# Optimization experiments

Hardware: AMD Instinct MI355X
Metric: run time of the kernel (lower is better)

The kernel has to match this reference:

```python
import jax, jax.numpy as jnp
import numpy as np

SIZE = (96, 160, 160)  # (D, H, W) from init_kwargs


def grid_sample_3d(inp, grid, padding_mode):
    """PyTorch-semantics 3D grid_sample, trilinear, align_corners=True.
    inp: (B, C, D, H, W); grid: (B, Do, Ho, Wo, 3) with grid[...,0]=x(W), [...,1]=y(H), [...,2]=z(D).
    """
    B, C, D, H, W = inp.shape
    x = (grid[..., 0] + 1.0) * 0.5 * (W - 1)
    y = (grid[..., 1] + 1.0) * 0.5 * (H - 1)
    z = (grid[..., 2] + 1.0) * 0.5 * (D - 1)
    if padding_mode == 'border':
        x = jnp.clip(x, 0.0, W - 1)
        y = jnp.clip(y, 0.0, H - 1)
        z = jnp.clip(z, 0.0, D - 1)
    x0f, y0f, z0f = jnp.floor(x), jnp.floor(y), jnp.floor(z)
    fx, fy, fz = x - x0f, y - y0f, z - z0f
    x0, y0, z0 = x0f.astype(jnp.int32), y0f.astype(jnp.int32), z0f.astype(jnp.int32)
    x1, y1, z1 = x0 + 1, y0 + 1, z0 + 1

    flat = inp.reshape(B, C, D * H * W)
    Do, Ho, Wo = grid.shape[1:4]
    N = Do * Ho * Wo

    def corner(zi, yi, xi, w):
        if padding_mode == 'zeros':
            valid = ((zi >= 0) & (zi < D) & (yi >= 0) & (yi < H) & (xi >= 0) & (xi < W))
            w = w * valid.astype(inp.dtype)
        zi = jnp.clip(zi, 0, D - 1)
        yi = jnp.clip(yi, 0, H - 1)
        xi = jnp.clip(xi, 0, W - 1)
        idx = ((zi * H + yi) * W + xi).reshape(B, 1, N)
        vals = jnp.take_along_axis(flat, idx, axis=2).reshape(B, C, Do, Ho, Wo)
        return vals * w[:, None]

    out = (corner(z0, y0, x0, (1 - fz) * (1 - fy) * (1 - fx))
           + corner(z0, y0, x1, (1 - fz) * (1 - fy) * fx)
           + corner(z0, y1, x0, (1 - fz) * fy * (1 - fx))
           + corner(z0, y1, x1, (1 - fz) * fy * fx)
           + corner(z1, y0, x0, fz * (1 - fy) * (1 - fx))
           + corner(z1, y0, x1, fz * (1 - fy) * fx)
           + corner(z1, y1, x0, fz * fy * (1 - fx))
           + corner(z1, y1, x1, fz * fy * fx))
    return out


def make_grid():
    D, H, W = SIZE
    g = jnp.stack(jnp.meshgrid(jnp.arange(D), jnp.arange(H), jnp.arange(W), indexing='ij'))
    return g[None].astype(jnp.float32)  # (1, 3, D, H, W)


def setup_inputs() -> dict:
    key = jax.random.key(0)
    k1, k2 = jax.random.split(key)
    D, H, W = SIZE
    src = jax.random.normal(k1, (1, 1, D, H, W), dtype=jnp.float32)
    flows = jax.random.normal(k2, (3, 1, 3, D, H, W), dtype=jnp.float32)
    range_flow = jnp.float32(0.4)
    return {"src": src, "flows": flows, "range_flow": range_flow}


def reference(src, flows, range_flow):
    D, H, W = SIZE
    grid = make_grid()  # (1, 3, D, H, W)
    shape = jnp.array([D, H, W], dtype=jnp.float32).reshape(-1, 1, 1, 1)
    acc = jnp.zeros_like(grid)
    for i in range(flows.shape[0]):  # small fixed number of flow stages
        flow = flows[i]
        ng = 2.0 * (grid / shape) - 1.0
        warped = grid_sample_3d(flow, jnp.transpose(ng, (0, 2, 3, 4, 1)), 'border')
        acc = acc + warped
    final = grid + acc * range_flow
    denom = jnp.array([D - 1, H - 1, W - 1], dtype=jnp.float32).reshape(-1, 1, 1, 1)
    final = 2.0 * (final / denom - 0.5)
    fg = jnp.transpose(final, (0, 2, 3, 4, 1))
    return grid_sample_3d(src, fg, 'zeros')
```

## Files before the change

kernel.cpp:

```cpp
#include <hip/hip_runtime.h>
#include <stdint.h>

constexpr int Dz = 96, Hy = 160, Wx = 160;
constexpr int NVOX = Dz * Hy * Wx;

constexpr int ZW = 6, YW = 3, XP = 56;
constexpr int ROWS = ZW * YW;
constexpr int NCHUNK = ROWS * 14;
constexpr int UI = 4;
constexpr int WBUF = UI * 64 * 4;

typedef __attribute__((address_space(3))) float lds_f;
typedef __attribute__((address_space(1))) const void gbl_v;

#define WAIT_VM(N)  do { asm volatile("s_waitcnt vmcnt(" #N ")" ::: "memory"); \
                         __builtin_amdgcn_sched_barrier(0); } while (0)
#define WAIT_LGKM() do { asm volatile("s_waitcnt lgkmcnt(0)" ::: "memory"); \
                         __builtin_amdgcn_sched_barrier(0); } while (0)

__global__ __launch_bounds__(128) void st_fused_kernel(
    const float* __restrict__ src,
    const float* __restrict__ flows,
    const float* __restrict__ rfp,
    float* __restrict__ out)
{
    __shared__ float raw[2][2][WBUF];
    const int t = threadIdx.x;
    const int v = t >> 6;
    const int lane = t & 63;

    const int bid = blockIdx.x;
    const int swz = (bid & 7) * 300 + (bid >> 3);
    const int wid = swz * 2 + v;
    const int wt = wid % 20;
    const int rest = wid / 20;
    const int dt = rest % 3;
    const int hp = rest / 3;
    const int w0w = wt * 8, d0 = dt * 32, h0 = hp * 2;
    const float rf = *rfp;

    const int Z0w = (19 * w0w) >> 5;
    const int X0 = 53 * dt;
    const int X0a = X0 & ~3;
    const int YB = (159 * h0) / 160;

    const char* ap[UI];
    {
        const char* fb = (const char*)flows + ((size_t)YB * Wx + X0a) * 4;
#pragma unroll
        for (int u = 0; u < UI; ++u) {
            int c = u * 64 + lane;
            if (c >= NCHUNK) c = NCHUNK - 1;
            int row = c / 14, ch = c - row * 14;
            int zr = row / 3, yr = row - zr * 3;
            ap[u] = fb + ((size_t)((Z0w + zr) * Hy + yr) * Wx) * 4 + ch * 16;
        }
    }

    auto issue_loads = [&](int buf) {
        lds_f* lb = (lds_f*)&raw[v][buf][0];
#pragma unroll
        for (int u = 0; u < UI; ++u)
            __builtin_amdgcn_global_load_lds((gbl_v*)ap[u], lb + u * 256, 16, 0, 0);
#pragma unroll
        for (int u = 0; u < UI; ++u) ap[u] += (size_t)NVOX * 4;
    };

    const int dl = lane & 31;
    const int half = lane >> 5;
    const int d = d0 + dl;

    const float xf = (float)(53 * d) * (1.0f / 32.0f);
    const int   x0i = (int)xf;
    const float fx  = xf - (float)x0i;
    const int   xx  = x0i - X0a;
    const float wxa = 1.0f - fx, wxb = fx;

    int rowoff[4];
    float wkz[4][4];
    {
        int zzk[4]; float wz0k[4], wz1k[4];
#pragma unroll
        for (int k = 0; k < 4; ++k) {
            const int w = w0w + 4 * half + k;
            const float zf = (float)(19 * w) * (1.0f / 32.0f);
            const int z0i = (int)zf;
            const float fz = zf - (float)z0i;
            zzk[k] = z0i - Z0w;
            wz0k[k] = 1.0f - fz; wz1k[k] = fz;
        }
        const int zz0 = zzk[0];
#pragma unroll
        for (int r = 0; r < 4; ++r) {
            rowoff[r] = min(zz0 + r, ZW - 1) * (YW * XP);
#pragma unroll
            for (int k = 0; k < 4; ++k) {
                const int rel = zzk[k] - zz0;
                wkz[r][k] = (rel == r) ? wz0k[k] : ((rel == r - 1) ? wz1k[k] : 0.0f);
            }
        }
    }

    float wyr[2][3];
#pragma unroll
    for (int j = 0; j < 2; ++j) {
        const int h = h0 + j;
        const float yf = (float)h * (159.0f / 160.0f);
        const int y0i = (int)yf;
        const float fy = yf - (float)y0i;
        const int yrel = y0i - YB;
        const float a = 1.0f - fy, b = fy;
        wyr[j][0] = (yrel == 0) ? a : 0.0f;
        wyr[j][1] = (yrel == 0) ? b : a;
        wyr[j][2] = (yrel == 0) ? 0.0f : b;
    }

    auto compute = [&](const float* lb, float (&acc)[4][2]) {
#pragma unroll
        for (int yy = 0; yy < 3; ++yy) {
            float zv0 = 0.f, zv1 = 0.f, zv2 = 0.f, zv3 = 0.f;
#pragma unroll
            for (int r = 0; r < 4; ++r) {
                const float* p = lb + rowoff[r] + yy * XP + xx;
                const float xv = wxa * p[0] + wxb * p[1];
                zv0 += wkz[r][0] * xv;
                zv1 += wkz[r][1] * xv;
                zv2 += wkz[r][2] * xv;
                zv3 += wkz[r][3] * xv;
            }
            acc[0][0] += wyr[0][yy] * zv0; acc[0][1] += wyr[1][yy] * zv0;
            acc[1][0] += wyr[0][yy] * zv1; acc[1][1] += wyr[1][yy] * zv1;
            acc[2][0] += wyr[0][yy] * zv2; acc[2][1] += wyr[1][yy] * zv2;
            acc[3][0] += wyr[0][yy] * zv3; acc[3][1] += wyr[1][yy] * zv3;
        }
    };

    float accA[4][2], accB[4][2], accC[4][2];
#pragma unroll
    for (int k = 0; k < 4; ++k)
#pragma unroll
        for (int j = 0; j < 2; ++j) { accA[k][j] = 0.f; accB[k][j] = 0.f; accC[k][j] = 0.f; }

    issue_loads(0);
    issue_loads(1);
    int cur = 0;

#pragma unroll 1
    for (int i = 0; i < 2; ++i) {
        WAIT_VM(4);
        compute(&raw[v][cur][0], accA);
        issue_loads(cur); cur ^= 1;

        WAIT_VM(4);
        compute(&raw[v][cur][0], accB);
        issue_loads(cur); cur ^= 1;

        WAIT_VM(4);
        compute(&raw[v][cur][0], accC);
        issue_loads(cur); cur ^= 1;
    }
    WAIT_VM(4);
    compute(&raw[v][cur][0], accA);
    issue_loads(cur); cur ^= 1;
    WAIT_VM(4);
    compute(&raw[v][cur][0], accB);
    cur ^= 1;
    WAIT_VM(0);
    compute(&raw[v][cur][0], accC);

    float* tr = &raw[v][0][0];
#pragma unroll
    for (int j = 0; j < 2; ++j) {
        const int h = h0 + j;
#pragma unroll
        for (int k = 0; k < 4; ++k) {
            const int w = w0w + 4 * half + k;
            const float f0 = (float)d + accA[k][j] * rf;
            const float f1 = (float)h + accB[k][j] * rf;
            const float f2 = (float)w + accC[k][j] * rf;

            const float xs = f0 * (159.0f / 95.0f);
            const float ys = f1;
            const float zs = f2 * (95.0f / 159.0f);

            const float xf0 = floorf(xs), yf0 = floorf(ys), zf0 = floorf(zs);
            const float gx = xs - xf0, gy = ys - yf0, gz = zs - zf0;
            const int xi0 = (int)xf0, yi0 = (int)yf0, zi0 = (int)zf0;

            const int xc = min(max(xi0, 0), Wx - 2);
            const bool sx0 = (xi0 == xc);
            const float wx0m = ((unsigned)xi0 < (unsigned)Wx) ? (1.0f - gx) : 0.0f;
            const float wx1m = ((unsigned)(xi0 + 1) < (unsigned)Wx) ? gx : 0.0f;

            const int yc0 = min(max(yi0, 0), Hy - 1);
            const int yc1 = min(max(yi0 + 1, 0), Hy - 1);
            const int zc0 = min(max(zi0, 0), Dz - 1);
            const int zc1 = min(max(zi0 + 1, 0), Dz - 1);
            const float wy0m = ((unsigned)yi0 < (unsigned)Hy) ? (1.0f - gy) : 0.0f;
            const float wy1m = ((unsigned)(yi0 + 1) < (unsigned)Hy) ? gy : 0.0f;
            const float wz0m = ((unsigned)zi0 < (unsigned)Dz) ? (1.0f - gz) : 0.0f;
            const float wz1m = ((unsigned)(zi0 + 1) < (unsigned)Dz) ? gz : 0.0f;

            const float w00 = wz0m * wy0m, w01 = wz0m * wy1m;
            const float w10 = wz1m * wy0m, w11 = wz1m * wy1m;

            float r = 0.0f;
            auto rowadd = [&](int zc, int yc, float wt) {
                const float* p = src + ((size_t)zc * Hy + yc) * Wx + xc;
                const float va = p[0], vb = p[1];
                const float s0 = sx0 ? va : vb;
                const float s1 = sx0 ? vb : va;
                r += wt * (wx0m * s0 + wx1m * s1);
            };
            rowadd(zc0, yc0, w00);
            rowadd(zc0, yc1, w01);
            rowadd(zc1, yc0, w10);
            rowadd(zc1, yc1, w11);

            tr[j * 288 + dl * 9 + 4 * half + k] = r;
        }
    }
    WAIT_LGKM();

    const int rrow = lane >> 3;
    const int rcol = lane & 7;
#pragma unroll
    for (int j = 0; j < 2; ++j)
#pragma unroll
        for (int m = 0; m < 4; ++m) {
            const int dr = m * 8 + rrow;
            out[((size_t)(d0 + dr) * Hy + (h0 + j)) * Wx + (w0w + rcol)] =
                tr[j * 288 + dr * 9 + rcol];
        }
}

extern "C" void kernel_launch(void* const* d_in, const int* in_sizes, int n_in,
                              void* d_out, int out_size, void* d_ws, size_t ws_size,
                              hipStream_t stream) {
    const float* src   = (const float*)d_in[0];
    const float* flows = (const float*)d_in[1];
    const float* rfp   = (const float*)d_in[2];
    float* out = (float*)d_out;

    st_fused_kernel<<<dim3(2400), 128, 0, stream>>>(src, flows, rfp, out);
}
```

Baseline: 31.44 us.

## Pre-sum flow stages in registers before interpolation, single LDS buffer

```diff
diff --git a/kernel.cpp b/kernel.cpp
--- a/kernel.cpp
+++ b/kernel.cpp
@@ -10,13 +10,9 @@
 constexpr int UI = 4;
 constexpr int WBUF = UI * 64 * 4;
 
-typedef __attribute__((address_space(3))) float lds_f;
-typedef __attribute__((address_space(1))) const void gbl_v;
-
-#define WAIT_VM(N)  do { asm volatile("s_waitcnt vmcnt(" #N ")" ::: "memory"); \
-                         __builtin_amdgcn_sched_barrier(0); } while (0)
 #define WAIT_LGKM() do { asm volatile("s_waitcnt lgkmcnt(0)" ::: "memory"); \
                          __builtin_amdgcn_sched_barrier(0); } while (0)
+#define FENCE() __builtin_amdgcn_sched_barrier(0)
 
 __global__ __launch_bounds__(128) void st_fused_kernel(
     const float* __restrict__ src,
@@ -24,7 +20,7 @@
     const float* __restrict__ rfp,
     float* __restrict__ out)
 {
-    __shared__ float raw[2][2][WBUF];
+    __shared__ float raw[2][WBUF];
     const int t = threadIdx.x;
     const int v = t >> 6;
     const int lane = t & 63;
@@ -57,13 +53,28 @@
         }
     }
 
-    auto issue_loads = [&](int buf) {
-        lds_f* lb = (lds_f*)&raw[v][buf][0];
-#pragma unroll
-        for (int u = 0; u < UI; ++u)
-            __builtin_amdgcn_global_load_lds((gbl_v*)ap[u], lb + u * 256, 16, 0, 0);
+    float4 nxt[3][UI];
+    auto issue_ch = [&]() {
+#pragma unroll
+        for (int i = 0; i < 3; ++i)
+#pragma unroll
+            for (int u = 0; u < UI; ++u)
+                nxt[i][u] = *(const float4*)(ap[u] + (size_t)i * (3u * NVOX * 4u));
 #pragma unroll
         for (int u = 0; u < UI; ++u) ap[u] += (size_t)NVOX * 4;
+    };
+    float* const lb = &raw[v][0];
+    auto commit_ch = [&]() {
+        float4* lb4 = (float4*)lb;
+#pragma unroll
+        for (int u = 0; u < UI; ++u) {
+            float4 s;
+            s.x = (nxt[0][u].x + nxt[1][u].x) + nxt[2][u].x;
+            s.y = (nxt[0][u].y + nxt[1][u].y) + nxt[2][u].y;
+            s.z = (nxt[0][u].z + nxt[1][u].z) + nxt[2][u].z;
+            s.w = (nxt[0][u].w + nxt[1][u].w) + nxt[2][u].w;
+            lb4[u * 64 + lane] = s;
+        }
     };
 
     const int dl = lane & 31;
@@ -115,7 +126,7 @@
         wyr[j][2] = (yrel == 0) ? 0.0f : b;
     }
 
-    auto compute = [&](const float* lb, float (&acc)[4][2]) {
+    auto compute = [&](float (&acc)[4][2]) {
 #pragma unroll
         for (int yy = 0; yy < 3; ++yy) {
             float zv0 = 0.f, zv1 = 0.f, zv2 = 0.f, zv3 = 0.f;
@@ -141,34 +152,19 @@
 #pragma unroll
         for (int j = 0; j < 2; ++j) { accA[k][j] = 0.f; accB[k][j] = 0.f; accC[k][j] = 0.f; }
 
-    issue_loads(0);
-    issue_loads(1);
-    int cur = 0;
-
-#pragma unroll 1
-    for (int i = 0; i < 2; ++i) {
-        WAIT_VM(4);
-        compute(&raw[v][cur][0], accA);
-        issue_loads(cur); cur ^= 1;
-
-        WAIT_VM(4);
-        compute(&raw[v][cur][0], accB);
-        issue_loads(cur); cur ^= 1;
-
-        WAIT_VM(4);
-        compute(&raw[v][cur][0], accC);
-        issue_loads(cur); cur ^= 1;
-    }
-    WAIT_VM(4);
-    compute(&raw[v][cur][0], accA);
-    issue_loads(cur); cur ^= 1;
-    WAIT_VM(4);
-    compute(&raw[v][cur][0], accB);
-    cur ^= 1;
-    WAIT_VM(0);
-    compute(&raw[v][cur][0], accC);
-
-    float* tr = &raw[v][0][0];
+    issue_ch();
+    commit_ch();
+    issue_ch();
+    compute(accA);
+    FENCE();
+    commit_ch();
+    issue_ch();
+    compute(accB);
+    FENCE();
+    commit_ch();
+    compute(accC);
+
+    float* tr = &raw[v][0];
 #pragma unroll
     for (int j = 0; j < 2; ++j) {
         const int h = h0 + j;
```

Result: faster. 30.20 us (-3.9%).
